# Kernel tuning notes

Measured on AMD Instinct MI355X. Metric: run time of the kernel, lower is better.

Reference implementation:

```python
import jax, jax.numpy as jnp
import numpy as np

N = 100000      # points
M = 12500       # cluster centers
E0 = 1600000    # point-level edges
E1 = 400000     # cluster-level edges
F_IN = 4        # raw point feature dim (e.g. intensity + extras)
D = 64          # hidden feature width
N_CLASSES = 8


def setup_inputs() -> dict:
    key = jax.random.key(0)
    ks = jax.random.split(key, 20)
    s = 0.05
    d = {}
    d["features"] = jax.random.normal(ks[0], (N, F_IN), jnp.float32)
    d["points"] = jax.random.normal(ks[1], (N, 3), jnp.float32)
    d["cluster_centers"] = jax.random.normal(ks[2], (M, 3), jnp.float32)
    d["l0_edges"] = jax.random.randint(ks[3], (E0, 2), 0, N)
    d["l1_edges"] = jax.random.randint(ks[4], (E1, 2), 0, M)
    d["labels"] = jax.random.randint(ks[5], (N,), 0, M)
    # Feature_extract MLP
    d["W_fe"] = s * jax.random.normal(ks[6], (F_IN + 3, D), jnp.float32)
    d["b_fe"] = jnp.zeros((D,), jnp.float32)
    # 4 Mini_GNN layers (layer2, layer2_1, layer6, layer6_1), stacked
    d["mini_We"] = s * jax.random.normal(ks[7], (4, D + 3, D), jnp.float32)
    d["mini_be"] = jnp.zeros((4, D), jnp.float32)
    d["mini_Wu"] = s * jax.random.normal(ks[8], (4, D, D), jnp.float32)
    d["mini_bu"] = jnp.zeros((4, D), jnp.float32)
    # Mini_to_Large
    d["W_m1"] = s * jax.random.normal(ks[9], (D + 3, D), jnp.float32)
    d["b_m1"] = jnp.zeros((D,), jnp.float32)
    d["W_m2"] = s * jax.random.normal(ks[10], (D, D), jnp.float32)
    d["b_m2"] = jnp.zeros((D,), jnp.float32)
    # 2 GNN layers on cluster graph (layer4, layer4_1), stacked
    d["gnn_We"] = s * jax.random.normal(ks[11], (2, D + 3, D), jnp.float32)
    d["gnn_be"] = jnp.zeros((2, D), jnp.float32)
    d["gnn_Wu"] = s * jax.random.normal(ks[12], (2, D, D), jnp.float32)
    d["gnn_bu"] = jnp.zeros((2, D), jnp.float32)
    # Large_to_Mini
    d["W_l"] = s * jax.random.normal(ks[13], (D + 3, D), jnp.float32)
    d["b_l"] = jnp.zeros((D,), jnp.float32)
    # Classifier
    d["W_c"] = s * jax.random.normal(ks[14], (D, N_CLASSES), jnp.float32)
    d["b_c"] = jnp.zeros((N_CLASSES,), jnp.float32)
    return d


def _gnn_layer(feat, pos, edges, We, be, Wu, bu, n_nodes):
    """PointGNN-style layer: gather -> edge MLP -> scatter max -> update MLP -> residual."""
    src, dst = edges[:, 0], edges[:, 1]
    e_in = jnp.concatenate([pos[src] - pos[dst], feat[src]], axis=-1)  # [E, 3+D]
    h = jax.nn.relu(e_in @ We + be)                                     # [E, D]
    agg = jax.ops.segment_max(h, dst, num_segments=n_nodes)            # [n, D]
    agg = jnp.where(jnp.isneginf(agg), 0.0, agg)  # nodes with no in-edges -> 0
    return jax.nn.relu(agg @ Wu + bu) + feat


def reference(features, points, cluster_centers, l0_edges, l1_edges, labels,
              W_fe, b_fe, mini_We, mini_be, mini_Wu, mini_bu,
              W_m1, b_m1, W_m2, b_m2, gnn_We, gnn_be, gnn_Wu, gnn_bu,
              W_l, b_l, W_c, b_c):
    rel = points - cluster_centers[labels]  # [N, 3] point pos relative to its cluster
    # layer1: Feature_extract
    f1 = jax.nn.relu(jnp.concatenate([features, rel], -1) @ W_fe + b_fe)
    # layer2 / layer2_1: Mini_GNN (scatter max) on point graph
    f2 = _gnn_layer(f1, points, l0_edges, mini_We[0], mini_be[0], mini_Wu[0], mini_bu[0], N)
    f2_1 = _gnn_layer(f2, points, l0_edges, mini_We[1], mini_be[1], mini_Wu[1], mini_bu[1], N)
    # layer3: Mini_to_Large (scatter sum by labels)
    h = jax.nn.relu(jnp.concatenate([f2_1, rel], -1) @ W_m1 + b_m1)
    c = jax.ops.segment_sum(h, labels, num_segments=M)  # [M, D]
    f3 = jax.nn.relu(c @ W_m2 + b_m2)
    # layer4 / layer4_1: GNN (scatter max) on cluster graph
    f4 = _gnn_layer(f3, cluster_centers, l1_edges, gnn_We[0], gnn_be[0], gnn_Wu[0], gnn_bu[0], M)
    f4_1 = _gnn_layer(f4, cluster_centers, l1_edges, gnn_We[1], gnn_be[1], gnn_Wu[1], gnn_bu[1], M)
    # layer5: Large_to_Mini (gather by labels)
    f5 = jax.nn.relu(jnp.concatenate([f4_1[labels], rel], -1) @ W_l + b_l)
    # layer6 / layer6_1 with residual skips per call()
    f6 = _gnn_layer(f5, points, l0_edges, mini_We[2], mini_be[2], mini_Wu[2], mini_bu[2], N)
    f6 = f6 + f2_1
    f6_1 = _gnn_layer(f6, points, l0_edges, mini_We[3], mini_be[3], mini_Wu[3], mini_bu[3], N)
    final = f6_1 + f2
    return final @ W_c + b_c  # [N, N_CLASSES] per-point logits
```

## Files before the change

kernel.cpp:

```cpp
#include <hip/hip_runtime.h>


#define N_PTS   100000
#define M_CL    12500
#define E0_N    1600000
#define E1_N    400000

#define NB      256
#define BIN_CAP 32
#define RANGE0  391
#define RANGE1  49
#define BCAP0   8192
#define BCAP1   2048
#define BCAPL   1024

#define LSTR    72

typedef unsigned short ushortT;
typedef short  short8 __attribute__((ext_vector_type(8)));
typedef short  s4v    __attribute__((ext_vector_type(4)));
typedef float  v4f    __attribute__((ext_vector_type(4)));
typedef _Float16 h2   __attribute__((ext_vector_type(2)));
typedef unsigned u4v  __attribute__((ext_vector_type(4)));

__device__ inline ushortT f2bf(float x){
  union{float f; unsigned u;} v; v.f = x;
  unsigned r = v.u + 0x7fffu + ((v.u >> 16) & 1u);
  return (ushortT)(r >> 16);
}
__device__ inline float bf2f(ushortT h){
  union{unsigned u; float f;} v; v.u = ((unsigned)h) << 16;
  return v.f;
}
__device__ inline ushortT f2h(float x){
  union{_Float16 h; ushortT u;} v; v.h = (_Float16)x;
  return v.u;
}
__device__ inline float h2f(ushortT u){
  union{ushortT u; _Float16 h;} v; v.u = u;
  return (float)v.h;
}
__device__ inline h2 pkmax(h2 a, h2 b){ return __builtin_elementwise_max(a, b); }
__device__ inline h2 u2h(unsigned u){ union{unsigned u; h2 h;} v{u}; return v.h; }


struct WSrc { const float* p[22]; };

__global__ __launch_bounds__(256) void k_init_wprep(WSrc s, ushortT* __restrict__ wt, ushortT* __restrict__ wtc,
                                                    float* __restrict__ wpp,
                                                    int* c0, int* c1, int* cL){
  int blk = blockIdx.x;
  if (blk == 0){
    int t = threadIdx.x;
    c0[t] = t*BCAP0; c1[t] = t*BCAP1; cL[t] = t*BCAPL;
    return;
  }
  int slot = blk - 1;
  if (slot < 15){
    const float* src = s.p[slot];
    ushortT* dst = wt + slot*4096;
    for (int e=threadIdx.x; e<4096; e+=256){
      int nn = e>>6, p = e&63;
      int kk = (p&3)*16 + (p>>2);
      dst[e] = f2bf(src[kk*64+nn]);
    }
  } else if (slot == 15){
    const float* src = s.p[15];
    for (int e=threadIdx.x; e<1024; e+=256){
      int nn = e>>6, p = e&63;
      int kk = (p&3)*16 + (p>>2);
      wtc[e] = (nn<8) ? f2bf(src[kk*8+nn]) : (ushortT)0;
    }
  } else {
    for (int e=threadIdx.x; e<6*192; e+=256){
      int i = e/192, rem = e - i*192, r = rem>>6, p = rem&63;
      wpp[e] = s.p[16+i][r*64 + ((p&3)*16 + (p>>2))];
    }
  }
}


template<int RANGE, bool LAB>
__device__ void bin_seg(const int* __restrict__ edges, int E,
                        int* __restrict__ bcur, unsigned* __restrict__ tmp,
                        int bid, int nblk,
                        unsigned* stage, int* scnt, int* sbase){
  int tid = threadIdx.x;
  int nchunks = (E + 2047) / 2048;
  for (int c = bid; c < nchunks; c += nblk){
    int base = c*2048;
    scnt[tid] = 0;
    __syncthreads();
    #pragma unroll
    for (int r=0;r<8;++r){
      int e = base + r*256 + tid;
      if (e < E){
        int s, d;
        if (LAB){ s = e; d = edges[e]; }
        else    { s = edges[2*e]; d = edges[2*e+1]; }
        int bk = d / RANGE;
        unsigned packed = ((unsigned)s << 11) | (unsigned)(d - bk*RANGE);
        int pos = atomicAdd(&scnt[bk], 1);
        if (pos < BIN_CAP) stage[bk*BIN_CAP+pos] = packed;
        else tmp[atomicAdd(&bcur[bk],1)] = packed;
      }
    }
    __syncthreads();
    {
      int nfl = scnt[tid]; if (nfl > BIN_CAP) nfl = BIN_CAP;
      sbase[tid] = atomicAdd(&bcur[tid], nfl);
    }
    __syncthreads();
    int wv = tid >> 6, ln = tid & 63;
    for (int bb=0; bb<32; ++bb){
      int bk = wv*64 + bb*2 + (ln>>5);
      int ent = ln & 31;
      int nf = scnt[bk]; if (nf > BIN_CAP) nf = BIN_CAP;
      if (ent < nf) tmp[sbase[bk]+ent] = stage[bk*BIN_CAP+ent];
    }
    __syncthreads();
  }
}

__global__ void k_scan_all(const int* c0, int* bb0, int* e0,
                           const int* c1, int* bb1, int* e1,
                           const int* cL, int* bbL, int* eL){
  const int* cur; int* bb; int* offe; int BC;
  if (blockIdx.x == 0){ cur=c0; bb=bb0; offe=e0; BC=BCAP0; }
  else if (blockIdx.x == 1){ cur=c1; bb=bb1; offe=e1; BC=BCAP1; }
  else { cur=cL; bb=bbL; offe=eL; BC=BCAPL; }
  int lane = threadIdx.x & 63;
  int base = lane*4;
  int v0 = cur[base+0] - (base+0)*BC;
  int v1 = cur[base+1] - (base+1)*BC;
  int v2 = cur[base+2] - (base+2)*BC;
  int v3 = cur[base+3] - (base+3)*BC;
  int psum = v0+v1+v2+v3, sc = psum;
  #pragma unroll
  for (int st=1; st<64; st<<=1){
    int x = __shfl_up(sc, st, 64);
    if (lane >= st) sc += x;
  }
  int ex = sc - psum;
  bb[base+0] = ex;
  bb[base+1] = ex + v0;
  bb[base+2] = ex + v0 + v1;
  bb[base+3] = ex + v0 + v1 + v2;
  if (lane == 63) *offe = sc;
}

template<int RANGE, int BCAP, int K>
__device__ void csr_build_seg(const unsigned* __restrict__ tmp, const int* __restrict__ bcur,
                              const int* __restrict__ bb, int n,
                              int* __restrict__ offs, int* __restrict__ csr,
                              int b, int* hist, int* part){
  int tid = threadIdx.x;
  int dlo = b*RANGE;
  int range = n - dlo; if (range > RANGE) range = RANGE; if (range < 0) range = 0;
  int cnt = bcur[b] - b*BCAP;
  for (int t=tid; t<RANGE; t+=256) hist[t] = 0;
  __syncthreads();
  const unsigned* sl = tmp + (size_t)b*BCAP;
  for (int j=tid; j<cnt; j+=256) atomicAdd(&hist[sl[j] & 2047u], 1);
  __syncthreads();
  int s = 0; int loc[K];
  #pragma unroll
  for (int kk=0; kk<K; ++kk){
    int idx = tid*K + kk;
    int v = (idx < RANGE) ? hist[idx] : 0;
    loc[kk] = s; s += v;
  }
  part[tid] = s; __syncthreads();
  int own = s;
  for (int st=1; st<256; st<<=1){
    int x = (tid >= st) ? part[tid-st] : 0;
    __syncthreads();
    part[tid] += x;
    __syncthreads();
  }
  int ebase = part[tid] - own;
  int gb = bb[b];
  __syncthreads();
  #pragma unroll
  for (int kk=0; kk<K; ++kk){
    int idx = tid*K + kk;
    if (idx < RANGE){
      int ex = ebase + loc[kk];
      if (idx < range) offs[dlo+idx] = gb + ex;
      hist[idx] = ex;
    }
  }
  __syncthreads();
  for (int j=tid; j<cnt; j+=256){
    unsigned p = sl[j];
    int pos = atomicAdd(&hist[p & 2047u], 1);
    csr[gb + pos] = (int)(p >> 11);
  }
}

__global__ __launch_bounds__(256) void k_build_all(
    const unsigned* t0, const int* bc0, const int* bb0, int* offs0, int* csr0,
    const unsigned* t1, const int* bc1, const int* bb1, int* offs1, int* csr1,
    const unsigned* tL, const int* bcL, const int* bbL, int* offsL, int* csrL){
  __shared__ int hist[RANGE0];
  __shared__ int part[256];
  int b = blockIdx.x;
  if (b < 256)      csr_build_seg<RANGE0,BCAP0,2>(t0, bc0, bb0, N_PTS, offs0, csr0, b, hist, part);
  else if (b < 512) csr_build_seg<RANGE1,BCAP1,1>(t1, bc1, bb1, M_CL, offs1, csr1, b-256, hist, part);
  else              csr_build_seg<RANGE1,BCAPL,1>(tL, bcL, bbL, M_CL, offsL, csrL, b-512, hist, part);
}


__global__ __launch_bounds__(256) void k_bin_f1g(
    const int* __restrict__ l0e, const int* __restrict__ l1e, const int* __restrict__ labels,
    int* bc0, int* bc1, int* bcL,
    unsigned* t0, unsigned* t1, unsigned* tL,
    const float* __restrict__ features, const float* __restrict__ points,
    const float* __restrict__ centers,
    const float* __restrict__ W, const float* __restrict__ bfe,
    const ushortT* __restrict__ Wt2, const float* __restrict__ bias2,
    const float* __restrict__ Wr2,
    float* __restrict__ rel, ushortT* __restrict__ f1b,
    ushortT* __restrict__ gout, int n, int ntiles, int nf1blk)
{
  __shared__ char smem[34816];
  int b = blockIdx.x;
  if (b < 501){
    unsigned* stage = (unsigned*)smem;
    int* scnt = (int*)(smem + 32768);
    int* sbase = (int*)(smem + 33792);
    if (b < 256)      bin_seg<RANGE0,false>(l0e, E0_N, bc0, t0, b, 256, stage, scnt, sbase);
    else if (b < 452) bin_seg<RANGE1,false>(l1e, E1_N, bc1, t1, b-256, 196, stage, scnt, sbase);
    else              bin_seg<RANGE1,true >(labels, N_PTS, bcL, tL, b-452, 49, stage, scnt, sbase);
    return;
  }
  ushortT* lds = (ushortT*)smem;
  int bb = b - 501;
  int tid = threadIdx.x;
  int lane = tid & 63, wslot = tid >> 6;
  int quad = lane >> 4, l15 = lane & 15;
  int permL = (lane & 15)*4 + (lane >> 4);
  int gw = (bb*256 + tid) >> 6;
  int nw = (nf1blk*256) >> 6;
  float Wf0=W[0*64+lane], Wf1=W[1*64+lane], Wf2=W[2*64+lane], Wf3=W[3*64+lane];
  float wr0=W[4*64+lane], wr1=W[5*64+lane], wr2=W[6*64+lane];
  float bias=bfe[lane];
  short8 s0_0 = *(const short8*)(Wt2 + ( 0 + l15)*64 +  0 + quad*8);
  short8 s0_1 = *(const short8*)(Wt2 + ( 0 + l15)*64 + 32 + quad*8);
  short8 s1_0 = *(const short8*)(Wt2 + (16 + l15)*64 +  0 + quad*8);
  short8 s1_1 = *(const short8*)(Wt2 + (16 + l15)*64 + 32 + quad*8);
  short8 s2_0 = *(const short8*)(Wt2 + (32 + l15)*64 +  0 + quad*8);
  short8 s2_1 = *(const short8*)(Wt2 + (32 + l15)*64 + 32 + quad*8);
  short8 s3_0 = *(const short8*)(Wt2 + (48 + l15)*64 +  0 + quad*8);
  short8 s3_1 = *(const short8*)(Wt2 + (48 + l15)*64 + 32 + quad*8);
  float eb0 = bias2[l15], eb1 = bias2[16+l15], eb2 = bias2[32+l15], eb3 = bias2[48+l15];
  float e0c0=Wr2[0*64+l15], e0c1=Wr2[0*64+16+l15], e0c2=Wr2[0*64+32+l15], e0c3=Wr2[0*64+48+l15];
  float e1c0=Wr2[1*64+l15], e1c1=Wr2[1*64+16+l15], e1c2=Wr2[1*64+32+l15], e1c3=Wr2[1*64+48+l15];
  float e2c0=Wr2[2*64+l15], e2c1=Wr2[2*64+16+l15], e2c2=Wr2[2*64+32+l15], e2c3=Wr2[2*64+48+l15];

  for (int t=gw; t<ntiles; t+=nw){
    int i0 = t*16;
    for (int r=0;r<16;++r){
      int row = i0 + r;
      bool ok = row < n;
      int rr = ok ? row : n-1;
      int lb = labels[rr];
      float rx = points[rr*3+0]-centers[lb*3+0];
      float ry = points[rr*3+1]-centers[lb*3+1];
      float rz = points[rr*3+2]-centers[lb*3+2];
      float acc = bias + wr0*rx + wr1*ry + wr2*rz;
      acc += features[rr*4+0]*Wf0 + features[rr*4+1]*Wf1;
      acc += features[rr*4+2]*Wf2 + features[rr*4+3]*Wf3;
      acc = fmaxf(acc, 0.f);
      ushortT ab = f2bf(acc);
      if (ok){
        f1b[(size_t)row*64 + permL] = ab;
        if (lane==0){ rel[row*3+0]=rx; rel[row*3+1]=ry; rel[row*3+2]=rz; }
      }
      lds[wslot*(16*LSTR) + r*LSTR + permL] = ab;
    }
    __builtin_amdgcn_wave_barrier();
    const ushortT* lp = lds + wslot*(16*LSTR) + l15*LSTR + quad*8;
    short8 sa0 = *(const short8*)(lp);
    short8 sa1 = *(const short8*)(lp + 32);
    __builtin_amdgcn_wave_barrier();
    v4f ec0 = {0.f,0.f,0.f,0.f}, ec1 = ec0, ec2 = ec0, ec3 = ec0;
    ec0 = __builtin_amdgcn_mfma_f32_16x16x32_bf16(sa0, s0_0, ec0, 0,0,0);
    ec1 = __builtin_amdgcn_mfma_f32_16x16x32_bf16(sa0, s1_0, ec1, 0,0,0);
    ec2 = __builtin_amdgcn_mfma_f32_16x16x32_bf16(sa0, s2_0, ec2, 0,0,0);
    ec3 = __builtin_amdgcn_mfma_f32_16x16x32_bf16(sa0, s3_0, ec3, 0,0,0);
    ec0 = __builtin_amdgcn_mfma_f32_16x16x32_bf16(sa1, s0_1, ec0, 0,0,0);
    ec1 = __builtin_amdgcn_mfma_f32_16x16x32_bf16(sa1, s1_1, ec1, 0,0,0);
    ec2 = __builtin_amdgcn_mfma_f32_16x16x32_bf16(sa1, s2_1, ec2, 0,0,0);
    ec3 = __builtin_amdgcn_mfma_f32_16x16x32_bf16(sa1, s3_1, ec3, 0,0,0);
    #pragma unroll
    for (int r=0;r<4;++r){
      int row = i0 + quad*4 + r;
      if (row < n){
        float vx=points[row*3+0], vy=points[row*3+1], vz=points[row*3+2];
        float g0 = ec0[r] + eb0 + vx*e0c0 + vy*e1c0 + vz*e2c0;
        float g1 = ec1[r] + eb1 + vx*e0c1 + vy*e1c1 + vz*e2c1;
        float g2 = ec2[r] + eb2 + vx*e0c2 + vy*e1c2 + vz*e2c2;
        float g3 = ec3[r] + eb3 + vx*e0c3 + vy*e1c3 + vz*e2c3;
        s4v o; o.x=(short)f2h(g0); o.y=(short)f2h(g1); o.z=(short)f2h(g2); o.w=(short)f2h(g3);
        *(s4v*)(gout + (size_t)row*64 + l15*4) = o;
      }
    }
  }
}


template<bool RELU, int NRES, bool USEREL, bool GATHER, bool OUT16, bool F16O, int EMODE, bool ERELU>
__global__ __launch_bounds__(256) void k_gemm(
    const ushortT* __restrict__ A, const ushortT* __restrict__ Wt,
    const float* __restrict__ bias, const float* __restrict__ Wr,
    const float* __restrict__ rel, const int* __restrict__ gidx,
    const ushortT* __restrict__ r1, const ushortT* __restrict__ r2,
    ushortT* __restrict__ out16,
    const ushortT* __restrict__ Wt2, const float* __restrict__ bias2,
    const float* __restrict__ Wr2, const float* __restrict__ vec2,
    void* __restrict__ eout,
    int n, int ntiles)
{
  constexpr int LDSZ = (EMODE>0) ? 4*16*LSTR : 4;
  __shared__ ushortT lds[LDSZ];
  int tid = threadIdx.x;
  int lane = tid & 63, wslot = tid >> 6;
  int quad = lane >> 4, l15 = lane & 15;
  int gw = (blockIdx.x*256 + tid) >> 6;
  int nw = (gridDim.x*256) >> 6;

  short8 bfr0_0 = *(const short8*)(Wt + ( 0 + l15)*64 +  0 + quad*8);
  short8 bfr0_1 = *(const short8*)(Wt + ( 0 + l15)*64 + 32 + quad*8);
  short8 bfr1_0 = *(const short8*)(Wt + (16 + l15)*64 +  0 + quad*8);
  short8 bfr1_1 = *(const short8*)(Wt + (16 + l15)*64 + 32 + quad*8);
  short8 bfr2_0 = *(const short8*)(Wt + (32 + l15)*64 +  0 + quad*8);
  short8 bfr2_1 = *(const short8*)(Wt + (32 + l15)*64 + 32 + quad*8);
  short8 bfr3_0 = *(const short8*)(Wt + (48 + l15)*64 +  0 + quad*8);
  short8 bfr3_1 = *(const short8*)(Wt + (48 + l15)*64 + 32 + quad*8);
  float bs0 = bias[ 0 + l15], bs1 = bias[16 + l15];
  float bs2 = bias[32 + l15], bs3 = bias[48 + l15];
  float w0c0=0,w0c1=0,w0c2=0,w0c3=0, w1c0=0,w1c1=0,w1c2=0,w1c3=0, w2c0=0,w2c1=0,w2c2=0,w2c3=0;
  if (USEREL){
    w0c0=Wr[0*64+l15]; w0c1=Wr[0*64+16+l15]; w0c2=Wr[0*64+32+l15]; w0c3=Wr[0*64+48+l15];
    w1c0=Wr[1*64+l15]; w1c1=Wr[1*64+16+l15]; w1c2=Wr[1*64+32+l15]; w1c3=Wr[1*64+48+l15];
    w2c0=Wr[2*64+l15]; w2c1=Wr[2*64+16+l15]; w2c2=Wr[2*64+32+l15]; w2c3=Wr[2*64+48+l15];
  }

  short8 s0_0{}, s0_1{}, s1_0{}, s1_1{}, s2_0{}, s2_1{}, s3_0{}, s3_1{};
  float eb0=0, eb1=0, eb2=0, eb3=0;
  float e0c0=0,e0c1=0,e0c2=0,e0c3=0, e1c0=0,e1c1=0,e1c2=0,e1c3=0, e2c0=0,e2c1=0,e2c2=0,e2c3=0;
  float ebias_c = 0.f;
  if (EMODE == 1){
    s0_0 = *(const short8*)(Wt2 + ( 0 + l15)*64 +  0 + quad*8);
    s0_1 = *(const short8*)(Wt2 + ( 0 + l15)*64 + 32 + quad*8);
    s1_0 = *(const short8*)(Wt2 + (16 + l15)*64 +  0 + quad*8);
    s1_1 = *(const short8*)(Wt2 + (16 + l15)*64 + 32 + quad*8);
    s2_0 = *(const short8*)(Wt2 + (32 + l15)*64 +  0 + quad*8);
    s2_1 = *(const short8*)(Wt2 + (32 + l15)*64 + 32 + quad*8);
    s3_0 = *(const short8*)(Wt2 + (48 + l15)*64 +  0 + quad*8);
    s3_1 = *(const short8*)(Wt2 + (48 + l15)*64 + 32 + quad*8);
    eb0 = bias2[l15]; eb1 = bias2[16+l15]; eb2 = bias2[32+l15]; eb3 = bias2[48+l15];
    e0c0=Wr2[0*64+l15]; e0c1=Wr2[0*64+16+l15]; e0c2=Wr2[0*64+32+l15]; e0c3=Wr2[0*64+48+l15];
    e1c0=Wr2[1*64+l15]; e1c1=Wr2[1*64+16+l15]; e1c2=Wr2[1*64+32+l15]; e1c3=Wr2[1*64+48+l15];
    e2c0=Wr2[2*64+l15]; e2c1=Wr2[2*64+16+l15]; e2c2=Wr2[2*64+32+l15]; e2c3=Wr2[2*64+48+l15];
  } else if (EMODE == 2){
    s0_0 = *(const short8*)(Wt2 + l15*64 +  0 + quad*8);
    s0_1 = *(const short8*)(Wt2 + l15*64 + 32 + quad*8);
    ebias_c = (l15 < 8) ? bias2[l15] : 0.f;
  }

  for (int t=gw; t<ntiles; t+=nw){
    int i0 = t*16;
    int rowA = i0 + l15; if (rowA >= n) rowA = n-1;
    if (GATHER) rowA = gidx[rowA];
    const ushortT* ap = A + (size_t)rowA*64 + quad*8;
    short8 a0 = *(const short8*)(ap);
    short8 a1 = *(const short8*)(ap + 32);
    v4f ac0 = {0.f,0.f,0.f,0.f}, ac1 = ac0, ac2 = ac0, ac3 = ac0;
    ac0 = __builtin_amdgcn_mfma_f32_16x16x32_bf16(a0, bfr0_0, ac0, 0,0,0);
    ac1 = __builtin_amdgcn_mfma_f32_16x16x32_bf16(a0, bfr1_0, ac1, 0,0,0);
    ac2 = __builtin_amdgcn_mfma_f32_16x16x32_bf16(a0, bfr2_0, ac2, 0,0,0);
    ac3 = __builtin_amdgcn_mfma_f32_16x16x32_bf16(a0, bfr3_0, ac3, 0,0,0);
    ac0 = __builtin_amdgcn_mfma_f32_16x16x32_bf16(a1, bfr0_1, ac0, 0,0,0);
    ac1 = __builtin_amdgcn_mfma_f32_16x16x32_bf16(a1, bfr1_1, ac1, 0,0,0);
    ac2 = __builtin_amdgcn_mfma_f32_16x16x32_bf16(a1, bfr2_1, ac2, 0,0,0);
    ac3 = __builtin_amdgcn_mfma_f32_16x16x32_bf16(a1, bfr3_1, ac3, 0,0,0);

    #pragma unroll
    for (int r=0;r<4;++r){
      int row = i0 + quad*4 + r;
      bool rowok = (row < n);
      float rx=0.f, ry=0.f, rz=0.f;
      if (USEREL && rowok){ rx=rel[row*3+0]; ry=rel[row*3+1]; rz=rel[row*3+2]; }
      float v0 = ac0[r] + bs0, v1 = ac1[r] + bs1, v2 = ac2[r] + bs2, v3 = ac3[r] + bs3;
      if (USEREL){
        v0 += rx*w0c0 + ry*w1c0 + rz*w2c0;
        v1 += rx*w0c1 + ry*w1c1 + rz*w2c1;
        v2 += rx*w0c2 + ry*w1c2 + rz*w2c2;
        v3 += rx*w0c3 + ry*w1c3 + rz*w2c3;
      }
      if (RELU){ v0=fmaxf(v0,0.f); v1=fmaxf(v1,0.f); v2=fmaxf(v2,0.f); v3=fmaxf(v3,0.f); }
      size_t pb = (size_t)row*64 + l15*4;
      if (rowok){
        if (NRES>=1){
          s4v rv = *(const s4v*)(r1 + pb);
          v0 += bf2f((ushortT)rv.x); v1 += bf2f((ushortT)rv.y);
          v2 += bf2f((ushortT)rv.z); v3 += bf2f((ushortT)rv.w);
        }
        if (NRES>=2){
          s4v rv = *(const s4v*)(r2 + pb);
          v0 += bf2f((ushortT)rv.x); v1 += bf2f((ushortT)rv.y);
          v2 += bf2f((ushortT)rv.z); v3 += bf2f((ushortT)rv.w);
        }
        if (OUT16){
          s4v o;
          if (F16O){ o.x=(short)f2h(v0); o.y=(short)f2h(v1); o.z=(short)f2h(v2); o.w=(short)f2h(v3); }
          else     { o.x=(short)f2bf(v0); o.y=(short)f2bf(v1); o.z=(short)f2bf(v2); o.w=(short)f2bf(v3); }
          *(s4v*)(out16 + pb) = o;
        }
      }
      if (EMODE > 0){
        int lb = wslot*(16*LSTR) + (quad*4+r)*LSTR + l15*4;
        s4v o; o.x=(short)f2bf(v0); o.y=(short)f2bf(v1); o.z=(short)f2bf(v2); o.w=(short)f2bf(v3);
        *(s4v*)(lds + lb) = o;
      }
    }

    if (EMODE > 0){
      __builtin_amdgcn_wave_barrier();
      const ushortT* lp = lds + wslot*(16*LSTR) + l15*LSTR + quad*8;
      short8 sa0 = *(const short8*)(lp);
      short8 sa1 = *(const short8*)(lp + 32);
      __builtin_amdgcn_wave_barrier();
      if (EMODE == 1){
        v4f ec0 = {0.f,0.f,0.f,0.f}, ec1 = ec0, ec2 = ec0, ec3 = ec0;
        ec0 = __builtin_amdgcn_mfma_f32_16x16x32_bf16(sa0, s0_0, ec0, 0,0,0);
        ec1 = __builtin_amdgcn_mfma_f32_16x16x32_bf16(sa0, s1_0, ec1, 0,0,0);
        ec2 = __builtin_amdgcn_mfma_f32_16x16x32_bf16(sa0, s2_0, ec2, 0,0,0);
        ec3 = __builtin_amdgcn_mfma_f32_16x16x32_bf16(sa0, s3_0, ec3, 0,0,0);
        ec0 = __builtin_amdgcn_mfma_f32_16x16x32_bf16(sa1, s0_1, ec0, 0,0,0);
        ec1 = __builtin_amdgcn_mfma_f32_16x16x32_bf16(sa1, s1_1, ec1, 0,0,0);
        ec2 = __builtin_amdgcn_mfma_f32_16x16x32_bf16(sa1, s2_1, ec2, 0,0,0);
        ec3 = __builtin_amdgcn_mfma_f32_16x16x32_bf16(sa1, s3_1, ec3, 0,0,0);
        ushortT* eo = (ushortT*)eout;
        #pragma unroll
        for (int r=0;r<4;++r){
          int row = i0 + quad*4 + r;
          if (row < n){
            float vx=vec2[row*3+0], vy=vec2[row*3+1], vz=vec2[row*3+2];
            float g0 = ec0[r] + eb0 + vx*e0c0 + vy*e1c0 + vz*e2c0;
            float g1 = ec1[r] + eb1 + vx*e0c1 + vy*e1c1 + vz*e2c1;
            float g2 = ec2[r] + eb2 + vx*e0c2 + vy*e1c2 + vz*e2c2;
            float g3 = ec3[r] + eb3 + vx*e0c3 + vy*e1c3 + vz*e2c3;
            if (ERELU){ g0=fmaxf(g0,0.f); g1=fmaxf(g1,0.f); g2=fmaxf(g2,0.f); g3=fmaxf(g3,0.f); }
            s4v o; o.x=(short)f2h(g0); o.y=(short)f2h(g1); o.z=(short)f2h(g2); o.w=(short)f2h(g3);
            *(s4v*)(eo + (size_t)row*64 + l15*4) = o;
          }
        }
      } else {
        v4f ec = {0.f,0.f,0.f,0.f};
        ec = __builtin_amdgcn_mfma_f32_16x16x32_bf16(sa0, s0_0, ec, 0,0,0);
        ec = __builtin_amdgcn_mfma_f32_16x16x32_bf16(sa1, s0_1, ec, 0,0,0);
        if (l15 < 8){
          float* eo = (float*)eout;
          #pragma unroll
          for (int r=0;r<4;++r){
            int row = i0 + quad*4 + r;
            if (row < n) eo[(size_t)row*8 + l15] = ec[r] + ebias_c;
          }
        }
      }
    }
  }
}


__global__ __launch_bounds__(256) void k_edge_agg(const int* __restrict__ offs, const int* __restrict__ csr,
                                                  const float* __restrict__ pos, const ushortT* __restrict__ g,
                                                  const float* __restrict__ Wp, ushortT* __restrict__ agg, int n){
  int lane = threadIdx.x & 63;
  int grp = lane >> 3, d8 = lane & 7;
  int gbase = lane & 56;
  int gw = (blockIdx.x*256 + threadIdx.x) >> 6;
  int nw = (gridDim.x*256) >> 6;
  const u4v* g4 = (const u4v*)g;
  float2 w0[4], w1[4], w2[4];
  #pragma unroll
  for (int q=0;q<4;++q){
    w0[q] = *(const float2*)(Wp + 0*64 + d8*8 + 2*q);
    w1[q] = *(const float2*)(Wp + 1*64 + d8*8 + 2*q);
    w2[q] = *(const float2*)(Wp + 2*64 + d8*8 + 2*q);
  }
  const h2 NEGBIG = {(_Float16)-60000.f, (_Float16)-60000.f};
  int n8 = (n+7) >> 3;
  for (int ii=gw; ii<n8; ii+=nw){
    int i0 = ii*8;
    int ig = i0 + grp; bool ok = ig < n; if (!ok) ig = n-1;
    int b = offs[ig], e = offs[ig+1];
    int cnt = e - b, c1 = cnt - 1;
    int mx = cnt;
    mx = max(mx, __shfl_xor(mx, 8, 64));
    mx = max(mx, __shfl_xor(mx, 16, 64));
    mx = max(mx, __shfl_xor(mx, 32, 64));
    h2 m0=NEGBIG, m1=NEGBIG, m2=NEGBIG, m3=NEGBIG;
    for (int J=0; J<mx; J+=8){
      if (J < cnt){
        int sv = csr[b + min(J + d8, c1)];
        #pragma unroll
        for (int jj=0; jj<8; ++jj){
          int s = __shfl(sv, gbase + jj, 64);
          u4v u = g4[(size_t)s*8 + d8];
          m0 = pkmax(m0, u2h(u.x));
          m1 = pkmax(m1, u2h(u.y));
          m2 = pkmax(m2, u2h(u.z));
          m3 = pkmax(m3, u2h(u.w));
        }
      }
    }
    float px = pos[ig*3+0], py = pos[ig*3+1], pz = pos[ig*3+2];
    u4v outv;
    {
      float sA = w0[0].x*px + w1[0].x*py + w2[0].x*pz;
      float sB = w0[0].y*px + w1[0].y*py + w2[0].y*pz;
      outv.x = (unsigned)f2bf(fmaxf((float)m0.x - sA, 0.f)) |
               ((unsigned)f2bf(fmaxf((float)m0.y - sB, 0.f)) << 16);
    }
    {
      float sA = w0[1].x*px + w1[1].x*py + w2[1].x*pz;
      float sB = w0[1].y*px + w1[1].y*py + w2[1].y*pz;
      outv.y = (unsigned)f2bf(fmaxf((float)m1.x - sA, 0.f)) |
               ((unsigned)f2bf(fmaxf((float)m1.y - sB, 0.f)) << 16);
    }
    {
      float sA = w0[2].x*px + w1[2].x*py + w2[2].x*pz;
      float sB = w0[2].y*px + w1[2].y*py + w2[2].y*pz;
      outv.z = (unsigned)f2bf(fmaxf((float)m2.x - sA, 0.f)) |
               ((unsigned)f2bf(fmaxf((float)m2.y - sB, 0.f)) << 16);
    }
    {
      float sA = w0[3].x*px + w1[3].x*py + w2[3].x*pz;
      float sB = w0[3].y*px + w1[3].y*py + w2[3].y*pz;
      outv.w = (unsigned)f2bf(fmaxf((float)m3.x - sA, 0.f)) |
               ((unsigned)f2bf(fmaxf((float)m3.y - sB, 0.f)) << 16);
    }
    if (ok) ((u4v*)agg)[(size_t)ig*8 + d8] = outv;
  }
}


__global__ __launch_bounds__(256) void k_seg_gather(const int* __restrict__ offs, const int* __restrict__ csr,
                                                    const ushortT* __restrict__ h, ushortT* __restrict__ c, int m){
  int lane = threadIdx.x & 63;
  int wv = (blockIdx.x*256 + threadIdx.x) >> 6;
  if (wv >= m) return;
  int b = offs[wv], e = offs[wv+1];
  float acc = 0.f;
  for (int k=b; k<e; ++k){
    int i = csr[k];
    acc += h2f(h[(size_t)i*64+lane]);
  }
  c[(size_t)wv*64+lane] = f2bf(acc);
}


extern "C" void kernel_launch(void* const* d_in, const int* in_sizes, int n_in,
                              void* d_out, int out_size, void* d_ws, size_t ws_size,
                              hipStream_t stream){
  const float* features = (const float*)d_in[0];
  const float* points   = (const float*)d_in[1];
  const float* centers  = (const float*)d_in[2];
  const int*   l0e      = (const int*)d_in[3];
  const int*   l1e      = (const int*)d_in[4];
  const int*   labels   = (const int*)d_in[5];
  const float* W_fe = (const float*)d_in[6];
  const float* b_fe = (const float*)d_in[7];
  const float* mWe  = (const float*)d_in[8];
  const float* mbe  = (const float*)d_in[9];
  const float* mWu  = (const float*)d_in[10];
  const float* mbu  = (const float*)d_in[11];
  const float* W_m1 = (const float*)d_in[12];
  const float* b_m1 = (const float*)d_in[13];
  const float* W_m2 = (const float*)d_in[14];
  const float* b_m2 = (const float*)d_in[15];
  const float* gWe  = (const float*)d_in[16];
  const float* gbe  = (const float*)d_in[17];
  const float* gWu  = (const float*)d_in[18];
  const float* gbu  = (const float*)d_in[19];
  const float* W_l  = (const float*)d_in[20];
  const float* b_l  = (const float*)d_in[21];
  const float* W_c  = (const float*)d_in[22];
  const float* b_c  = (const float*)d_in[23];
  float* out = (float*)d_out;

  char* w = (char*)d_ws;
  size_t off = 0;
  auto alloc = [&](size_t bytes)->void*{
    void* p = (void*)(w + off);
    off = (off + bytes + 255) & ~(size_t)255;
    return p;
  };
  float* rel  = (float*)alloc((size_t)N_PTS*3*4);
  ushortT* UF1 = (ushortT*)alloc((size_t)N_PTS*64*2);
  ushortT* UF2 = (ushortT*)alloc((size_t)N_PTS*64*2);
  ushortT* UF21= (ushortT*)alloc((size_t)N_PTS*64*2);
  ushortT* UF5 = (ushortT*)alloc((size_t)N_PTS*64*2);
  ushortT* UF6 = (ushortT*)alloc((size_t)N_PTS*64*2);
  ushortT* gbuf= (ushortT*)alloc((size_t)N_PTS*64*2);
  ushortT* abuf= (ushortT*)alloc((size_t)N_PTS*64*2);
  ushortT* cb_b= (ushortT*)alloc((size_t)M_CL*64*2);
  ushortT* UF3 = (ushortT*)alloc((size_t)M_CL*64*2);
  ushortT* UF4 = (ushortT*)alloc((size_t)M_CL*64*2);
  ushortT* cg_b= (ushortT*)alloc((size_t)M_CL*64*2);
  ushortT* cagg_b = (ushortT*)alloc((size_t)M_CL*64*2);
  ushortT* f41_b  = (ushortT*)alloc((size_t)M_CL*64*2);
  ushortT* wt  = (ushortT*)alloc((size_t)15*4096*2);
  ushortT* wtc = (ushortT*)alloc((size_t)1024*2);
  float* wpp = (float*)alloc((size_t)6*192*4);
  int* offs0 = (int*)alloc((size_t)(N_PTS+1)*4);
  int* csr0  = (int*)alloc((size_t)E0_N*4);
  int* offs1 = (int*)alloc((size_t)(M_CL+1)*4);
  int* csr1  = (int*)alloc((size_t)E1_N*4);
  int* offsL = (int*)alloc((size_t)(M_CL+1)*4);
  int* csrL  = (int*)alloc((size_t)N_PTS*4);
  unsigned* tmp0 = (unsigned*)alloc((size_t)NB*BCAP0*4);
  unsigned* tmp1 = (unsigned*)alloc((size_t)NB*BCAP1*4);
  unsigned* tmpL = (unsigned*)alloc((size_t)NB*BCAPL*4);
  int* bcur0 = (int*)alloc(NB*4);
  int* bcur1 = (int*)alloc(NB*4);
  int* bcurL = (int*)alloc(NB*4);
  int* bb0   = (int*)alloc(NB*4);
  int* bb1   = (int*)alloc(NB*4);
  int* bbL   = (int*)alloc(NB*4);
  (void)ws_size; (void)in_sizes; (void)n_in; (void)out_size;

  const int NT_N = (N_PTS+15)/16;
  const int NT_M = (M_CL +15)/16;
  const int GBG_N = 1563;
  const int GBG_M = 196;
  const int GB_N  = 3125;

  WSrc ws{};
  ws.p[0]=mWu+0*4096; ws.p[1]=mWu+1*4096; ws.p[2]=mWu+2*4096; ws.p[3]=mWu+3*4096;
  ws.p[4]=W_m2; ws.p[5]=gWu+0*4096; ws.p[6]=gWu+1*4096;
  ws.p[7]=mWe+0*4288+192; ws.p[8]=mWe+1*4288+192; ws.p[9]=mWe+2*4288+192; ws.p[10]=mWe+3*4288+192;
  ws.p[11]=W_m1; ws.p[12]=W_l; ws.p[13]=gWe+0*4288+192; ws.p[14]=gWe+1*4288+192;
  ws.p[15]=W_c;
  ws.p[16]=mWe+0*4288; ws.p[17]=mWe+1*4288; ws.p[18]=mWe+2*4288; ws.p[19]=mWe+3*4288;
  ws.p[20]=gWe+0*4288; ws.p[21]=gWe+1*4288;
  k_init_wprep<<<18, 256, 0, stream>>>(ws, wt, wtc, wpp, bcur0, bcur1, bcurL);
  k_bin_f1g<<<501 + GBG_N, 256, 0, stream>>>(l0e, l1e, labels, bcur0, bcur1, bcurL, tmp0, tmp1, tmpL,
      features, points, centers, W_fe, b_fe,
      wt+7*4096, mbe+0, mWe+0*4288, rel, UF1, gbuf, N_PTS, NT_N, GBG_N);
  k_scan_all<<<3, 64, 0, stream>>>(bcur0, bb0, offs0+N_PTS, bcur1, bb1, offs1+M_CL, bcurL, bbL, offsL+M_CL);
  k_build_all<<<768, 256, 0, stream>>>(tmp0, bcur0, bb0, offs0, csr0,
                                       tmp1, bcur1, bb1, offs1, csr1,
                                       tmpL, bcurL, bbL, offsL, csrL);

  k_edge_agg<<<GB_N,256,0,stream>>>(offs0, csr0, points, gbuf, wpp+0*192, abuf, N_PTS);
  k_gemm<true,1,false,false,true,false,1,false><<<GBG_N,256,0,stream>>>(abuf, wt+0*4096, mbu+0,
      nullptr, nullptr, nullptr, UF1, nullptr, UF2,
      wt+8*4096, mbe+64, mWe+1*4288, points, gbuf, N_PTS, NT_N);
  k_edge_agg<<<GB_N,256,0,stream>>>(offs0, csr0, points, gbuf, wpp+1*192, abuf, N_PTS);
  k_gemm<true,1,false,false,true,false,1,true><<<GBG_N,256,0,stream>>>(abuf, wt+1*4096, mbu+64,
      nullptr, nullptr, nullptr, UF2, nullptr, UF21,
      wt+11*4096, b_m1, W_m1+4096, rel, gbuf, N_PTS, NT_N);
  k_seg_gather<<<(M_CL*64+255)/256, 256, 0, stream>>>(offsL, csrL, gbuf, cb_b, M_CL);
  k_gemm<true,0,false,false,true,false,1,false><<<GBG_M,256,0,stream>>>(cb_b, wt+4*4096, b_m2,
      nullptr, nullptr, nullptr, nullptr, nullptr, UF3,
      wt+13*4096, gbe+0, gWe+0*4288, centers, cg_b, M_CL, NT_M);
  k_edge_agg<<<GBG_M,256,0,stream>>>(offs1, csr1, centers, cg_b, wpp+4*192, cagg_b, M_CL);
  k_gemm<true,1,false,false,true,false,1,false><<<GBG_M,256,0,stream>>>(cagg_b, wt+5*4096, gbu+0,
      nullptr, nullptr, nullptr, UF3, nullptr, UF4,
      wt+14*4096, gbe+64, gWe+1*4288, centers, cg_b, M_CL, NT_M);
  k_edge_agg<<<GBG_M,256,0,stream>>>(offs1, csr1, centers, cg_b, wpp+5*192, cagg_b, M_CL);
  k_gemm<true,1,false,false,true,false,0,false><<<GBG_M,256,0,stream>>>(cagg_b, wt+6*4096, gbu+64,
      nullptr, nullptr, nullptr, UF4, nullptr, f41_b,
      nullptr, nullptr, nullptr, nullptr, nullptr, M_CL, NT_M);
  k_gemm<true,0,true,true,true,false,1,false><<<GBG_N,256,0,stream>>>(f41_b, wt+12*4096, b_l,
      W_l+4096, rel, labels, nullptr, nullptr, UF5,
      wt+9*4096, mbe+128, mWe+2*4288, points, gbuf, N_PTS, NT_N);
  k_edge_agg<<<GB_N,256,0,stream>>>(offs0, csr0, points, gbuf, wpp+2*192, abuf, N_PTS);
  k_gemm<true,2,false,false,true,false,1,false><<<GBG_N,256,0,stream>>>(abuf, wt+2*4096, mbu+128,
      nullptr, nullptr, nullptr, UF5, UF21, UF6,
      wt+10*4096, mbe+192, mWe+3*4288, points, gbuf, N_PTS, NT_N);
  k_edge_agg<<<GB_N,256,0,stream>>>(offs0, csr0, points, gbuf, wpp+3*192, abuf, N_PTS);
  k_gemm<true,2,false,false,false,false,2,false><<<GBG_N,256,0,stream>>>(abuf, wt+3*4096, mbu+192,
      nullptr, nullptr, nullptr, UF6, UF2, nullptr,
      wtc, b_c, nullptr, nullptr, out, N_PTS, NT_N);
}
```

Before: 460.3 us.

## Fold bin-base scan into CSR build kernel and shrink staging bins

Result: no change. 459.4 us (-0.2%).

```diff
diff --git a/kernel.cpp b/kernel.cpp
--- a/kernel.cpp
+++ b/kernel.cpp
@@ -7,7 +7,7 @@
 #define E1_N    400000
 
 #define NB      256
-#define BIN_CAP 32
+#define BIN_CAP 16
 #define RANGE0  391
 #define RANGE1  49
 #define BCAP0   8192
@@ -112,9 +112,9 @@
     }
     __syncthreads();
     int wv = tid >> 6, ln = tid & 63;
-    for (int bb=0; bb<32; ++bb){
-      int bk = wv*64 + bb*2 + (ln>>5);
-      int ent = ln & 31;
+    for (int bb=0; bb<16; ++bb){
+      int bk = wv*64 + bb*4 + (ln>>4);
+      int ent = ln & 15;
       int nf = scnt[bk]; if (nf > BIN_CAP) nf = BIN_CAP;
       if (ent < nf) tmp[sbase[bk]+ent] = stage[bk*BIN_CAP+ent];
     }
@@ -122,42 +122,26 @@
   }
 }
 
-__global__ void k_scan_all(const int* c0, int* bb0, int* e0,
-                           const int* c1, int* bb1, int* e1,
-                           const int* cL, int* bbL, int* eL){
-  const int* cur; int* bb; int* offe; int BC;
-  if (blockIdx.x == 0){ cur=c0; bb=bb0; offe=e0; BC=BCAP0; }
-  else if (blockIdx.x == 1){ cur=c1; bb=bb1; offe=e1; BC=BCAP1; }
-  else { cur=cL; bb=bbL; offe=eL; BC=BCAPL; }
-  int lane = threadIdx.x & 63;
-  int base = lane*4;
-  int v0 = cur[base+0] - (base+0)*BC;
-  int v1 = cur[base+1] - (base+1)*BC;
-  int v2 = cur[base+2] - (base+2)*BC;
-  int v3 = cur[base+3] - (base+3)*BC;
-  int psum = v0+v1+v2+v3, sc = psum;
-  #pragma unroll
-  for (int st=1; st<64; st<<=1){
-    int x = __shfl_up(sc, st, 64);
-    if (lane >= st) sc += x;
-  }
-  int ex = sc - psum;
-  bb[base+0] = ex;
-  bb[base+1] = ex + v0;
-  bb[base+2] = ex + v0 + v1;
-  bb[base+3] = ex + v0 + v1 + v2;
-  if (lane == 63) *offe = sc;
-}
-
 template<int RANGE, int BCAP, int K>
 __device__ void csr_build_seg(const unsigned* __restrict__ tmp, const int* __restrict__ bcur,
-                              const int* __restrict__ bb, int n,
-                              int* __restrict__ offs, int* __restrict__ csr,
+                              int n, int* __restrict__ offs, int* __restrict__ csr,
                               int b, int* hist, int* part){
   int tid = threadIdx.x;
   int dlo = b*RANGE;
   int range = n - dlo; if (range > RANGE) range = RANGE; if (range < 0) range = 0;
   int cnt = bcur[b] - b*BCAP;
+  part[tid] = bcur[tid] - tid*BCAP;
+  __syncthreads();
+  for (int st=1; st<256; st<<=1){
+    int x = (tid >= st) ? part[tid-st] : 0;
+    __syncthreads();
+    part[tid] += x;
+    __syncthreads();
+  }
+  int gb = part[b] - cnt;
+  int total = part[NB-1];
+  if (b == NB-1 && tid == 0) offs[n] = total;
+  __syncthreads();
   for (int t=tid; t<RANGE; t+=256) hist[t] = 0;
   __syncthreads();
   const unsigned* sl = tmp + (size_t)b*BCAP;
@@ -179,7 +163,6 @@
     __syncthreads();
   }
   int ebase = part[tid] - own;
-  int gb = bb[b];
   __syncthreads();
   #pragma unroll
   for (int kk=0; kk<K; ++kk){
@@ -199,15 +182,15 @@
 }
 
 __global__ __launch_bounds__(256) void k_build_all(
-    const unsigned* t0, const int* bc0, const int* bb0, int* offs0, int* csr0,
-    const unsigned* t1, const int* bc1, const int* bb1, int* offs1, int* csr1,
-    const unsigned* tL, const int* bcL, const int* bbL, int* offsL, int* csrL){
+    const unsigned* t0, const int* bc0, int* offs0, int* csr0,
+    const unsigned* t1, const int* bc1, int* offs1, int* csr1,
+    const unsigned* tL, const int* bcL, int* offsL, int* csrL){
   __shared__ int hist[RANGE0];
   __shared__ int part[256];
   int b = blockIdx.x;
-  if (b < 256)      csr_build_seg<RANGE0,BCAP0,2>(t0, bc0, bb0, N_PTS, offs0, csr0, b, hist, part);
-  else if (b < 512) csr_build_seg<RANGE1,BCAP1,1>(t1, bc1, bb1, M_CL, offs1, csr1, b-256, hist, part);
-  else              csr_build_seg<RANGE1,BCAPL,1>(tL, bcL, bbL, M_CL, offsL, csrL, b-512, hist, part);
+  if (b < 256)      csr_build_seg<RANGE0,BCAP0,2>(t0, bc0, N_PTS, offs0, csr0, b, hist, part);
+  else if (b < 512) csr_build_seg<RANGE1,BCAP1,1>(t1, bc1, M_CL, offs1, csr1, b-256, hist, part);
+  else              csr_build_seg<RANGE1,BCAPL,1>(tL, bcL, M_CL, offsL, csrL, b-512, hist, part);
 }
 
 
@@ -223,12 +206,12 @@
     float* __restrict__ rel, ushortT* __restrict__ f1b,
     ushortT* __restrict__ gout, int n, int ntiles, int nf1blk)
 {
-  __shared__ char smem[34816];
+  __shared__ char smem[18432];
   int b = blockIdx.x;
   if (b < 501){
     unsigned* stage = (unsigned*)smem;
-    int* scnt = (int*)(smem + 32768);
-    int* sbase = (int*)(smem + 33792);
+    int* scnt = (int*)(smem + 16384);
+    int* sbase = (int*)(smem + 17408);
     if (b < 256)      bin_seg<RANGE0,false>(l0e, E0_N, bc0, t0, b, 256, stage, scnt, sbase);
     else if (b < 452) bin_seg<RANGE1,false>(l1e, E1_N, bc1, t1, b-256, 196, stage, scnt, sbase);
     else              bin_seg<RANGE1,true >(labels, N_PTS, bcL, tL, b-452, 49, stage, scnt, sbase);
@@ -629,9 +612,6 @@
   int* bcur0 = (int*)alloc(NB*4);
   int* bcur1 = (int*)alloc(NB*4);
   int* bcurL = (int*)alloc(NB*4);
-  int* bb0   = (int*)alloc(NB*4);
-  int* bb1   = (int*)alloc(NB*4);
-  int* bbL   = (int*)alloc(NB*4);
   (void)ws_size; (void)in_sizes; (void)n_in; (void)out_size;
 
   const int NT_N = (N_PTS+15)/16;
@@ -652,10 +632,9 @@
   k_bin_f1g<<<501 + GBG_N, 256, 0, stream>>>(l0e, l1e, labels, bcur0, bcur1, bcurL, tmp0, tmp1, tmpL,
       features, points, centers, W_fe, b_fe,
       wt+7*4096, mbe+0, mWe+0*4288, rel, UF1, gbuf, N_PTS, NT_N, GBG_N);
-  k_scan_all<<<3, 64, 0, stream>>>(bcur0, bb0, offs0+N_PTS, bcur1, bb1, offs1+M_CL, bcurL, bbL, offsL+M_CL);
-  k_build_all<<<768, 256, 0, stream>>>(tmp0, bcur0, bb0, offs0, csr0,
-                                       tmp1, bcur1, bb1, offs1, csr1,
-                                       tmpL, bcurL, bbL, offsL, csrL);
+  k_build_all<<<768, 256, 0, stream>>>(tmp0, bcur0, offs0, csr0,
+                                       tmp1, bcur1, offs1, csr1,
+                                       tmpL, bcurL, offsL, csrL);
 
   k_edge_agg<<<GB_N,256,0,stream>>>(offs0, csr0, points, gbuf, wpp+0*192, abuf, N_PTS);
   k_gemm<true,1,false,false,true,false,1,false><<<GBG_N,256,0,stream>>>(abuf, wt+0*4096, mbu+0,
```
